# Optimization experiments

Hardware: AMD Instinct MI355X
Metric: run time of the kernel (lower is better)

## Reference

```python
import jax, jax.numpy as jnp
import numpy as np

N = 50000      # original nodes
DEG = 8        # regular out-degree
E = N * DEG    # edges
K = 2          # bloom factor per node
C = 25000      # clusters (new nodes)
D_IN = 128
D_OUT = 128
D_BLOOM = 16   # (lmax+1)^2, lmax=3
D_INTER = D_BLOOM + D_OUT


def seg_mean(vals, idx, num):
    # scatter_mean: segment_sum / counts (clipped to 1)
    s = jax.ops.segment_sum(vals, idx, num_segments=num)
    cnt = jax.ops.segment_sum(jnp.ones((idx.shape[0], 1), vals.dtype), idx, num_segments=num)
    return s / jnp.maximum(cnt, 1.0)


def setup_inputs() -> dict:
    key = jax.random.key(0)
    ks = jax.random.split(key, 10)
    x = jax.random.normal(ks[0], (N, D_IN), jnp.float32)
    pos = jax.random.normal(ks[1], (N, 3), jnp.float32)
    src = jnp.repeat(jnp.arange(N, dtype=jnp.int32), DEG)          # regular out-degree
    dst = jax.random.randint(ks[2], (E,), 0, N, jnp.int32)
    edge_index = jnp.stack([src, dst], axis=0)
    edge_attr = jax.random.normal(ks[3], (E, 3), jnp.float32)      # relative-position features
    batch = jnp.zeros((N,), jnp.int32)                              # single graph
    clusters = jax.random.randint(ks[4], (N * K,), 0, C, jnp.int32) # cluster assignment of bloom nodes
    W_conv = jax.random.normal(ks[5], (D_IN, D_INTER), jnp.float32) * 0.05
    W_cedge = jax.random.normal(ks[6], (3, D_INTER), jnp.float32) * 0.05
    W_bloom = jax.random.normal(ks[7], (D_BLOOM, K * 3), jnp.float32) * 0.05
    W_gather = jax.random.normal(ks[8], (D_OUT, D_OUT), jnp.float32) * 0.05
    W_gedge = jax.random.normal(ks[9], (3, D_OUT), jnp.float32) * 0.05
    return {"x": x, "pos": pos, "edge_index": edge_index, "edge_attr": edge_attr,
            "batch": batch, "clusters": clusters, "W_conv": W_conv, "W_cedge": W_cedge,
            "W_bloom": W_bloom, "W_gather": W_gather, "W_gedge": W_gedge}


def reference(x, pos, edge_index, edge_attr, batch, clusters,
              W_conv, W_cedge, W_bloom, W_gather, W_gedge):
    src, dst = edge_index[0], edge_index[1]
    # bloom conv: edge messages -> mean aggregate on destination
    msg = x[src] @ W_conv + edge_attr @ W_cedge                    # [E, D_INTER]
    out = seg_mean(msg, dst, N)                                    # [N, D_INTER]
    sph, h = out[:, :D_BLOOM], out[:, D_BLOOM:]
    # bloom-expand: each node emits K bloomed points
    bloom_batch = jnp.repeat(jnp.arange(N, dtype=jnp.int32), K)    # [N*K]
    bloom_pos = (pos[:, None, :] + (sph @ W_bloom).reshape(N, K, 3)).reshape(N * K, 3)
    # (bloom_pos feeds the external clusterer; `clusters` is its precomputed output)
    pos_b = pos[bloom_batch]                                       # [N*K, 3]
    new_pos = seg_mean(pos_b, clusters, C)                         # scatter_mean pool -> [C, 3]
    # gather conv over edges bloom-node -> cluster
    g_attr = pos_b - new_pos[clusters]                             # [N*K, 3]
    gmsg = h[bloom_batch] @ W_gather + g_attr @ W_gedge            # [N*K, D_OUT]
    x_new = seg_mean(gmsg, clusters, C)                            # [C, D_OUT]
    # new_edge_index: spspmm chain. For each original edge (a->b), node b's bloom
    # nodes map to clusters; clusters sharing a common neighbor a become connected.
    cb = clusters.reshape(N, K)[dst].reshape(N, DEG * K)           # [N, deg*K] (regular degree)
    dK = DEG * K
    ns = jnp.broadcast_to(cb[:, :, None], (N, dK, dK)).reshape(-1)
    nd = jnp.broadcast_to(cb[:, None, :], (N, dK, dK)).reshape(-1)
    enc = ns * C + nd                                              # fits int32 (C*C < 2^31)
    enc = jnp.unique(enc, size=enc.shape[0], fill_value=0)         # dedup like spspmm (padded with 0)
    new_edge_index = jnp.stack([enc // C, enc % C], axis=0)
    new_edge_attr = new_pos[new_edge_index[1]] - new_pos[new_edge_index[0]]
    return (x_new, new_pos, new_edge_index, new_edge_attr)
```

## Files before the change

kernel.cpp:

```cpp
#include <hip/hip_runtime.h>
#include <hip/hip_bf16.h>
#include <stdint.h>

#define N_NODES   50000
#define N_EDGES   400000
#define NK        100000
#define C_CL      25000
#define TOTE      12800000
#define CHUNK_BITS 18
#define NCHUNK    2385
#define HIST_BLOCKS 782

__global__ __launch_bounds__(256) void mm128(const float* __restrict__ A, int lda,
                                             const float* __restrict__ B, int ldb, int bcol0,
                                             float* __restrict__ out, int rows) {
    int t = blockIdx.x * 256 + threadIdx.x;
    int r = t >> 5;
    int c = (t & 31) << 2;
    if (r >= rows) return;
    const float* Ar = A + (size_t)r * lda;
    const float* Bc = B + bcol0 + c;
    float4 acc = make_float4(0.f, 0.f, 0.f, 0.f);
#pragma unroll
    for (int k = 0; k < 128; k += 4) {
        float4 a  = *(const float4*)(Ar + k);
        float4 b0 = *(const float4*)(Bc + (size_t)(k + 0) * ldb);
        float4 b1 = *(const float4*)(Bc + (size_t)(k + 1) * ldb);
        float4 b2 = *(const float4*)(Bc + (size_t)(k + 2) * ldb);
        float4 b3 = *(const float4*)(Bc + (size_t)(k + 3) * ldb);
        acc.x += a.x * b0.x + a.y * b1.x + a.z * b2.x + a.w * b3.x;
        acc.y += a.x * b0.y + a.y * b1.y + a.z * b2.y + a.w * b3.y;
        acc.z += a.x * b0.z + a.y * b1.z + a.z * b2.z + a.w * b3.z;
        acc.w += a.x * b0.w + a.y * b1.w + a.z * b2.w + a.w * b3.w;
    }
    *(float4*)(out + (size_t)r * 128 + c) = acc;
}

__global__ __launch_bounds__(256) void hist_idx(const int* __restrict__ idx, int n, int* __restrict__ cnt) {
    int i = blockIdx.x * 256 + threadIdx.x;
    if (i < n) atomicAdd(&cnt[idx[i]], 1);
}

__global__ __launch_bounds__(256) void reduce_blk(const int* __restrict__ v, int n, int* __restrict__ bsum) {
    __shared__ int s[256];
    int t = threadIdx.x;
    int i = blockIdx.x * 256 + t;
    s[t] = (i < n) ? v[i] : 0;
    __syncthreads();
    for (int o = 128; o > 0; o >>= 1) { if (t < o) s[t] += s[t + o]; __syncthreads(); }
    if (t == 0) bsum[blockIdx.x] = s[0];
}

__global__ __launch_bounds__(256) void scan_small(int* data, int n, int* total_out) {
    __shared__ int s[256];
    __shared__ int carry;
    int t = threadIdx.x;
    if (t == 0) carry = 0;
    __syncthreads();
    for (int base = 0; base < n; base += 256) {
        int i = base + t;
        int v = (i < n) ? data[i] : 0;
        s[t] = v;
        __syncthreads();
        for (int o = 1; o < 256; o <<= 1) {
            int x = (t >= o) ? s[t - o] : 0;
            __syncthreads();
            s[t] += x;
            __syncthreads();
        }
        int inc = s[t];
        int tot = s[255];
        int cy  = carry;
        __syncthreads();
        if (i < n) data[i] = cy + inc - v;
        if (t == 0) carry = cy + tot;
        __syncthreads();
    }
    if (t == 0 && total_out) *total_out = carry;
}

__global__ __launch_bounds__(256) void scan_offs(const int* __restrict__ cnt, int n,
                                                 const int* __restrict__ bscan, int* __restrict__ offs) {
    __shared__ int s[256];
    int t = threadIdx.x;
    int i = blockIdx.x * 256 + t;
    int v = (i < n) ? cnt[i] : 0;
    s[t] = v;
    __syncthreads();
    for (int o = 1; o < 256; o <<= 1) {
        int x = (t >= o) ? s[t - o] : 0;
        __syncthreads();
        s[t] += x;
        __syncthreads();
    }
    if (i < n) offs[i] = bscan[blockIdx.x] + s[t] - v;
}

__global__ __launch_bounds__(256) void scatter_ids(const int* __restrict__ idx, int n,
                                                   int* __restrict__ cursors, int* __restrict__ ids) {
    int i = blockIdx.x * 256 + threadIdx.x;
    if (i < n) {
        int p = atomicAdd(&cursors[idx[i]], 1);
        ids[p] = i;
    }
}

__global__ __launch_bounds__(256) void gather_h(const float* __restrict__ y, const float* __restrict__ ea,
                                                const int* __restrict__ offs, const int* __restrict__ cnt,
                                                const int* __restrict__ eids, const float* __restrict__ Wce,
                                                float* __restrict__ h) {
    int l = threadIdx.x & 63;
    int n = blockIdx.x * 4 + (threadIdx.x >> 6);
    int off = offs[n], m = cnt[n];
    float ax = 0.f, ay = 0.f, ae = 0.f;
    for (int i = 0; i < m; ++i) {
        int e = eids[off + i];
        int s = e >> 3;
        float2 v = *(const float2*)(y + (size_t)s * 128 + 2 * l);
        ax += v.x; ay += v.y;
        if (l < 3) ae += ea[(size_t)e * 3 + l];
    }
    float e0 = __shfl(ae, 0), e1 = __shfl(ae, 1), e2 = __shfl(ae, 2);
    float inv = 1.f / (float)(m > 0 ? m : 1);
    int c0 = 2 * l, c1 = 2 * l + 1;
    float h0 = (ax + e0 * Wce[16 + c0] + e1 * Wce[144 + 16 + c0] + e2 * Wce[288 + 16 + c0]) * inv;
    float h1 = (ay + e0 * Wce[16 + c1] + e1 * Wce[144 + 16 + c1] + e2 * Wce[288 + 16 + c1]) * inv;
    *(float2*)(h + (size_t)n * 128 + 2 * l) = make_float2(h0, h1);
}

__global__ __launch_bounds__(256) void gather_out(const float* __restrict__ hW, const float* __restrict__ pos,
                                                  const int* __restrict__ offs2, const int* __restrict__ cnt2,
                                                  const int* __restrict__ bids,
                                                  float* __restrict__ xnew, float* __restrict__ newpos) {
    int l = threadIdx.x & 63;
    int c = blockIdx.x * 4 + (threadIdx.x >> 6);
    int off = offs2[c], m = cnt2[c];
    float ax = 0.f, ay = 0.f, ap = 0.f;
    for (int i = 0; i < m; ++i) {
        int b  = bids[off + i];
        int nd = b >> 1;
        float2 v = *(const float2*)(hW + (size_t)nd * 128 + 2 * l);
        ax += v.x; ay += v.y;
        if (l < 3) ap += pos[(size_t)nd * 3 + l];
    }
    float inv = 1.f / (float)(m > 0 ? m : 1);
    *(float2*)(xnew + (size_t)c * 128 + 2 * l) = make_float2(ax * inv, ay * inv);
    if (l < 3) newpos[(size_t)c * 3 + l] = ap * inv;
}

__global__ __launch_bounds__(256) void pair_hist(const int* __restrict__ dstA, const int* __restrict__ clu,
                                                 int* __restrict__ gcnt) {
    __shared__ int cb[64][16];
    __shared__ int hist[NCHUNK];
    int t = threadIdx.x;
    int n0 = blockIdx.x * 64;
    int nvalid = N_NODES - n0; if (nvalid > 64) nvalid = 64;
    for (int i = t; i < NCHUNK; i += 256) hist[i] = 0;
    for (int i = t; i < 1024; i += 256) {
        int ln = i >> 4, j = i & 15;
        if (ln < nvalid) {
            int d = dstA[(n0 + ln) * 8 + (j >> 1)];
            cb[ln][j] = clu[d * 2 + (j & 1)];
        }
    }
    __syncthreads();
#pragma unroll 4
    for (int q = 0; q < 64; ++q) {
        int idx = t * 64 + q;
        int ln = idx >> 8, p = idx & 255;
        if (ln < nvalid) {
            unsigned enc = (unsigned)cb[ln][p >> 4] * 25000u + (unsigned)cb[ln][p & 15];
            atomicAdd(&hist[enc >> CHUNK_BITS], 1);
        }
    }
    __syncthreads();
    for (int i = t; i < NCHUNK; i += 256) { int h = hist[i]; if (h) atomicAdd(&gcnt[i], h); }
}

__global__ __launch_bounds__(256) void pair_scatter(const int* __restrict__ dstA, const int* __restrict__ clu,
                                                    int* __restrict__ gcur, unsigned* __restrict__ pbuf) {
    __shared__ int cb[64][16];
    __shared__ int hist[NCHUNK];
    __shared__ int lcur[NCHUNK];
    int t = threadIdx.x;
    int n0 = blockIdx.x * 64;
    int nvalid = N_NODES - n0; if (nvalid > 64) nvalid = 64;
    for (int i = t; i < NCHUNK; i += 256) hist[i] = 0;
    for (int i = t; i < 1024; i += 256) {
        int ln = i >> 4, j = i & 15;
        if (ln < nvalid) {
            int d = dstA[(n0 + ln) * 8 + (j >> 1)];
            cb[ln][j] = clu[d * 2 + (j & 1)];
        }
    }
    __syncthreads();
#pragma unroll 4
    for (int q = 0; q < 64; ++q) {
        int idx = t * 64 + q;
        int ln = idx >> 8, p = idx & 255;
        if (ln < nvalid) {
            unsigned enc = (unsigned)cb[ln][p >> 4] * 25000u + (unsigned)cb[ln][p & 15];
            atomicAdd(&hist[enc >> CHUNK_BITS], 1);
        }
    }
    __syncthreads();
    for (int i = t; i < NCHUNK; i += 256) { int h = hist[i]; if (h) lcur[i] = atomicAdd(&gcur[i], h); }
    __syncthreads();
#pragma unroll 4
    for (int q = 0; q < 64; ++q) {
        int idx = t * 64 + q;
        int ln = idx >> 8, p = idx & 255;
        if (ln < nvalid) {
            unsigned enc = (unsigned)cb[ln][p >> 4] * 25000u + (unsigned)cb[ln][p & 15];
            int pos = atomicAdd(&lcur[enc >> CHUNK_BITS], 1);
            pbuf[pos] = enc;
        }
    }
}

__global__ __launch_bounds__(256) void chunk_count(const unsigned* __restrict__ pbuf,
                                                   const int* __restrict__ goffs, const int* __restrict__ gcnt,
                                                   int* __restrict__ ucnt) {
    __shared__ unsigned bm[8192];
    __shared__ int s[256];
    int t = threadIdx.x, c = blockIdx.x;
    for (int i = t; i < 8192; i += 256) bm[i] = 0;
    __syncthreads();
    int off = goffs[c], m = gcnt[c];
    unsigned basee = (unsigned)c << CHUNK_BITS;
    for (int i = t; i < m; i += 256) {
        unsigned e = pbuf[off + i] - basee;
        atomicOr(&bm[e >> 5], 1u << (e & 31));
    }
    __syncthreads();
    int acc = 0;
#pragma unroll
    for (int w = 0; w < 32; ++w) acc += __popc(bm[w * 256 + t]);
    s[t] = acc;
    __syncthreads();
    for (int o = 128; o > 0; o >>= 1) { if (t < o) s[t] += s[t + o]; __syncthreads(); }
    if (t == 0) ucnt[c] = s[0];
}

__global__ __launch_bounds__(256) void chunk_emit(const unsigned* __restrict__ pbuf,
                                                  const int* __restrict__ goffs, const int* __restrict__ gcnt,
                                                  const int* __restrict__ uoffs, const float* __restrict__ newpos,
                                                  float* __restrict__ ei0, float* __restrict__ ei1,
                                                  float* __restrict__ attr) {
    __shared__ unsigned bm[8192];
    __shared__ int wsum[32][4];
    int t = threadIdx.x, c = blockIdx.x;
    int lane = t & 63, wid = t >> 6;
    for (int i = t; i < 8192; i += 256) bm[i] = 0;
    __syncthreads();
    int off = goffs[c], m = gcnt[c];
    unsigned basee = (unsigned)c << CHUNK_BITS;
    for (int i = t; i < m; i += 256) {
        unsigned e = pbuf[off + i] - basee;
        atomicOr(&bm[e >> 5], 1u << (e & 31));
    }
    __syncthreads();
    int ubase = uoffs[c];
    int carry = 0;
    for (int g = 0; g < 32; ++g) {
        unsigned word = bm[g * 256 + t];
        int pc = __popc(word);
        int incl = pc;
#pragma unroll
        for (int o = 1; o < 64; o <<= 1) {
            int v = __shfl_up(incl, o, 64);
            if (lane >= o) incl += v;
        }
        if (lane == 63) wsum[g][wid] = incl;
        __syncthreads();
        int w0 = wsum[g][0], w1 = wsum[g][1], w2 = wsum[g][2], w3 = wsum[g][3];
        int wpre = (wid > 0 ? w0 : 0) + (wid > 1 ? w1 : 0) + (wid > 2 ? w2 : 0);
        int rank = ubase + carry + wpre + incl - pc;
        carry += w0 + w1 + w2 + w3;
        unsigned wbase = basee + (((unsigned)(g * 256 + t)) << 5);
        while (word) {
            int b = __ffs(word) - 1;
            word &= word - 1;
            unsigned v  = wbase + (unsigned)b;
            unsigned ns = v / 25000u;
            unsigned nd = v - ns * 25000u;
            ei0[rank] = (float)ns;
            ei1[rank] = (float)nd;
            float dx = newpos[nd * 3 + 0] - newpos[ns * 3 + 0];
            float dy = newpos[nd * 3 + 1] - newpos[ns * 3 + 1];
            float dz = newpos[nd * 3 + 2] - newpos[ns * 3 + 2];
            attr[(size_t)3 * rank + 0] = dx;
            attr[(size_t)3 * rank + 1] = dy;
            attr[(size_t)3 * rank + 2] = dz;
            ++rank;
        }
    }
}

__global__ __launch_bounds__(256) void tail_zero(const int* __restrict__ Uptr,
                                                 float* __restrict__ ei0, float* __restrict__ ei1,
                                                 float* __restrict__ attr) {
    int i = blockIdx.x * 256 + threadIdx.x;
    if (i >= TOTE) return;
    if (i >= *Uptr) {
        ei0[i] = 0.f;
        ei1[i] = 0.f;
        attr[(size_t)3 * i + 0] = 0.f;
        attr[(size_t)3 * i + 1] = 0.f;
        attr[(size_t)3 * i + 2] = 0.f;
    }
}

extern "C" void kernel_launch(void* const* d_in, const int* in_sizes, int n_in,
                              void* d_out, int out_size, void* d_ws, size_t ws_size,
                              hipStream_t stream) {
    const float* x     = (const float*)d_in[0];
    const float* pos   = (const float*)d_in[1];
    const int*   dstA  = (const int*)d_in[2] + N_EDGES;
    const float* ea    = (const float*)d_in[3];
    const int*   clu   = (const int*)d_in[5];
    const float* Wconv = (const float*)d_in[6];
    const float* Wce   = (const float*)d_in[7];
    const float* Wg    = (const float*)d_in[9];

    float* out_f  = (float*)d_out;
    float* xnew   = out_f;
    float* newpos = out_f + 3200000;
    float* ei0    = out_f + 3275000;
    float* ei1    = out_f + 16075000;
    float* attr   = out_f + 28875000;
    float* y      = attr;
    float* h      = attr + 6400000;
    float* hW     = y;

    uint8_t* w8 = (uint8_t*)d_ws;
    unsigned* pbuf = (unsigned*)(w8);
    int* cnt       = (int*)(w8 + 51200000);
    int* offs      = (int*)(w8 + 51400000);
    int* cursors   = (int*)(w8 + 51600000);
    int* eids      = (int*)(w8 + 51800000);
    int* cnt2      = (int*)(w8 + 53400000);
    int* offs2     = (int*)(w8 + 53500000);
    int* cursors2  = (int*)(w8 + 53600000);
    int* bids      = (int*)(w8 + 53700000);
    int* bsum      = (int*)(w8 + 54100000);
    int* gcnt      = (int*)(w8 + 54120480);
    int* goffs     = (int*)(w8 + 54130020);
    int* gcur      = (int*)(w8 + 54139560);
    int* ucnt      = (int*)(w8 + 54149100);
    int* uoffs     = (int*)(w8 + 54158640);
    int* Uptr      = (int*)(w8 + 54168180);

    hipMemsetAsync(gcnt, 0, NCHUNK * 4, stream);
    hipMemsetAsync(cnt,  0, N_NODES * 4, stream);
    hipMemsetAsync(cnt2, 0, C_CL * 4, stream);

    mm128<<<(N_NODES * 32) / 256, 256, 0, stream>>>(x, 128, Wconv, 144, 16, y, N_NODES);

    hist_idx<<<(N_EDGES + 255) / 256, 256, 0, stream>>>(dstA, N_EDGES, cnt);
    reduce_blk<<<196, 256, 0, stream>>>(cnt, N_NODES, bsum);
    scan_small<<<1, 256, 0, stream>>>(bsum, 196, nullptr);
    scan_offs<<<196, 256, 0, stream>>>(cnt, N_NODES, bsum, offs);
    hipMemcpyAsync(cursors, offs, N_NODES * 4, hipMemcpyDeviceToDevice, stream);
    scatter_ids<<<(N_EDGES + 255) / 256, 256, 0, stream>>>(dstA, N_EDGES, cursors, eids);

    gather_h<<<N_NODES / 4, 256, 0, stream>>>(y, ea, offs, cnt, eids, Wce, h);

    mm128<<<(N_NODES * 32) / 256, 256, 0, stream>>>(h, 128, Wg, 128, 0, hW, N_NODES);

    hist_idx<<<(NK + 255) / 256, 256, 0, stream>>>(clu, NK, cnt2);
    reduce_blk<<<98, 256, 0, stream>>>(cnt2, C_CL, bsum);
    scan_small<<<1, 256, 0, stream>>>(bsum, 98, nullptr);
    scan_offs<<<98, 256, 0, stream>>>(cnt2, C_CL, bsum, offs2);
    hipMemcpyAsync(cursors2, offs2, C_CL * 4, hipMemcpyDeviceToDevice, stream);
    scatter_ids<<<(NK + 255) / 256, 256, 0, stream>>>(clu, NK, cursors2, bids);

    gather_out<<<C_CL / 4, 256, 0, stream>>>(hW, pos, offs2, cnt2, bids, xnew, newpos);

    pair_hist<<<HIST_BLOCKS, 256, 0, stream>>>(dstA, clu, gcnt);
    hipMemcpyAsync(goffs, gcnt, NCHUNK * 4, hipMemcpyDeviceToDevice, stream);
    scan_small<<<1, 256, 0, stream>>>(goffs, NCHUNK, nullptr);
    hipMemcpyAsync(gcur, goffs, NCHUNK * 4, hipMemcpyDeviceToDevice, stream);
    pair_scatter<<<HIST_BLOCKS, 256, 0, stream>>>(dstA, clu, gcur, pbuf);
    chunk_count<<<NCHUNK, 256, 0, stream>>>(pbuf, goffs, gcnt, ucnt);
    hipMemcpyAsync(uoffs, ucnt, NCHUNK * 4, hipMemcpyDeviceToDevice, stream);
    scan_small<<<1, 256, 0, stream>>>(uoffs, NCHUNK, Uptr);
    chunk_emit<<<NCHUNK, 256, 0, stream>>>(pbuf, goffs, gcnt, uoffs, newpos, ei0, ei1, attr);
    tail_zero<<<TOTE / 256, 256, 0, stream>>>(Uptr, ei0, ei1, attr);

    (void)in_sizes; (void)n_in; (void)out_size; (void)ws_size;
}
```

Baseline: 1.127 ms.

## Prefold W_gather into conv weights and compact deduped edges in place

Precomputes W1 = Wconv_h·Wg and W2 = Wce_h·Wg in a small kernel, so one 128x128 matmul over x replaces the conv matmul plus the second matmul on h. This relies on the linearity of the mean aggregation. It also merges the count and emit bitmap passes into one compaction kernel that writes the unique keys back into pbuf, followed by a flat expand kernel. That avoids building the shared-memory bitmap twice per chunk, at the cost of an extra global write and read of the compacted keys and a small change in floating-point summation order.

```diff
diff --git a/kernel.cpp b/kernel.cpp
--- a/kernel.cpp
+++ b/kernel.cpp
@@ -11,15 +11,35 @@
 #define NCHUNK    2385
 #define HIST_BLOCKS 782
 
+__global__ __launch_bounds__(256) void fuse_w(const float* __restrict__ Wconv, const float* __restrict__ Wce,
+                                              const float* __restrict__ Wg,
+                                              float* __restrict__ W1, float* __restrict__ W2) {
+    int id = blockIdx.x * 256 + threadIdx.x;
+    int r = id >> 7, c = id & 127;
+    if (r >= 131) return;
+    float acc = 0.f;
+    if (r < 128) {
+        const float* wr = Wconv + r * 144 + 16;
+#pragma unroll 8
+        for (int j = 0; j < 128; ++j) acc += wr[j] * Wg[j * 128 + c];
+        W1[r * 128 + c] = acc;
+    } else {
+        const float* wr = Wce + (r - 128) * 144 + 16;
+#pragma unroll 8
+        for (int j = 0; j < 128; ++j) acc += wr[j] * Wg[j * 128 + c];
+        W2[(r - 128) * 128 + c] = acc;
+    }
+}
+
 __global__ __launch_bounds__(256) void mm128(const float* __restrict__ A, int lda,
-                                             const float* __restrict__ B, int ldb, int bcol0,
+                                             const float* __restrict__ B, int ldb,
                                              float* __restrict__ out, int rows) {
     int t = blockIdx.x * 256 + threadIdx.x;
     int r = t >> 5;
     int c = (t & 31) << 2;
     if (r >= rows) return;
     const float* Ar = A + (size_t)r * lda;
-    const float* Bc = B + bcol0 + c;
+    const float* Bc = B + c;
     float4 acc = make_float4(0.f, 0.f, 0.f, 0.f);
 #pragma unroll
     for (int k = 0; k < 128; k += 4) {
@@ -105,10 +125,10 @@
     }
 }
 
-__global__ __launch_bounds__(256) void gather_h(const float* __restrict__ y, const float* __restrict__ ea,
-                                                const int* __restrict__ offs, const int* __restrict__ cnt,
-                                                const int* __restrict__ eids, const float* __restrict__ Wce,
-                                                float* __restrict__ h) {
+__global__ __launch_bounds__(256) void gather_hW(const float* __restrict__ yW, const float* __restrict__ ea,
+                                                 const int* __restrict__ offs, const int* __restrict__ cnt,
+                                                 const int* __restrict__ eids, const float* __restrict__ W2,
+                                                 float* __restrict__ hW) {
     int l = threadIdx.x & 63;
     int n = blockIdx.x * 4 + (threadIdx.x >> 6);
     int off = offs[n], m = cnt[n];
@@ -116,16 +136,16 @@
     for (int i = 0; i < m; ++i) {
         int e = eids[off + i];
         int s = e >> 3;
-        float2 v = *(const float2*)(y + (size_t)s * 128 + 2 * l);
+        float2 v = *(const float2*)(yW + (size_t)s * 128 + 2 * l);
         ax += v.x; ay += v.y;
         if (l < 3) ae += ea[(size_t)e * 3 + l];
     }
     float e0 = __shfl(ae, 0), e1 = __shfl(ae, 1), e2 = __shfl(ae, 2);
     float inv = 1.f / (float)(m > 0 ? m : 1);
     int c0 = 2 * l, c1 = 2 * l + 1;
-    float h0 = (ax + e0 * Wce[16 + c0] + e1 * Wce[144 + 16 + c0] + e2 * Wce[288 + 16 + c0]) * inv;
-    float h1 = (ay + e0 * Wce[16 + c1] + e1 * Wce[144 + 16 + c1] + e2 * Wce[288 + 16 + c1]) * inv;
-    *(float2*)(h + (size_t)n * 128 + 2 * l) = make_float2(h0, h1);
+    float h0 = (ax + e0 * W2[c0] + e1 * W2[128 + c0] + e2 * W2[256 + c0]) * inv;
+    float h1 = (ay + e0 * W2[c1] + e1 * W2[128 + c1] + e2 * W2[256 + c1]) * inv;
+    *(float2*)(hW + (size_t)n * 128 + 2 * l) = make_float2(h0, h1);
 }
 
 __global__ __launch_bounds__(256) void gather_out(const float* __restrict__ hW, const float* __restrict__ pos,
@@ -218,12 +238,13 @@
     }
 }
 
-__global__ __launch_bounds__(256) void chunk_count(const unsigned* __restrict__ pbuf,
-                                                   const int* __restrict__ goffs, const int* __restrict__ gcnt,
-                                                   int* __restrict__ ucnt) {
+__global__ __launch_bounds__(256) void chunk_compact(unsigned* __restrict__ pbuf,
+                                                     const int* __restrict__ goffs, const int* __restrict__ gcnt,
+                                                     int* __restrict__ ucnt) {
     __shared__ unsigned bm[8192];
-    __shared__ int s[256];
+    __shared__ int wsum[32][4];
     int t = threadIdx.x, c = blockIdx.x;
+    int lane = t & 63, wid = t >> 6;
     for (int i = t; i < 8192; i += 256) bm[i] = 0;
     __syncthreads();
     int off = goffs[c], m = gcnt[c];
@@ -233,34 +254,6 @@
         atomicOr(&bm[e >> 5], 1u << (e & 31));
     }
     __syncthreads();
-    int acc = 0;
-#pragma unroll
-    for (int w = 0; w < 32; ++w) acc += __popc(bm[w * 256 + t]);
-    s[t] = acc;
-    __syncthreads();
-    for (int o = 128; o > 0; o >>= 1) { if (t < o) s[t] += s[t + o]; __syncthreads(); }
-    if (t == 0) ucnt[c] = s[0];
-}
-
-__global__ __launch_bounds__(256) void chunk_emit(const unsigned* __restrict__ pbuf,
-                                                  const int* __restrict__ goffs, const int* __restrict__ gcnt,
-                                                  const int* __restrict__ uoffs, const float* __restrict__ newpos,
-                                                  float* __restrict__ ei0, float* __restrict__ ei1,
-                                                  float* __restrict__ attr) {
-    __shared__ unsigned bm[8192];
-    __shared__ int wsum[32][4];
-    int t = threadIdx.x, c = blockIdx.x;
-    int lane = t & 63, wid = t >> 6;
-    for (int i = t; i < 8192; i += 256) bm[i] = 0;
-    __syncthreads();
-    int off = goffs[c], m = gcnt[c];
-    unsigned basee = (unsigned)c << CHUNK_BITS;
-    for (int i = t; i < m; i += 256) {
-        unsigned e = pbuf[off + i] - basee;
-        atomicOr(&bm[e >> 5], 1u << (e & 31));
-    }
-    __syncthreads();
-    int ubase = uoffs[c];
     int carry = 0;
     for (int g = 0; g < 32; ++g) {
         unsigned word = bm[g * 256 + t];
@@ -275,25 +268,38 @@
         __syncthreads();
         int w0 = wsum[g][0], w1 = wsum[g][1], w2 = wsum[g][2], w3 = wsum[g][3];
         int wpre = (wid > 0 ? w0 : 0) + (wid > 1 ? w1 : 0) + (wid > 2 ? w2 : 0);
-        int rank = ubase + carry + wpre + incl - pc;
+        int rank = off + carry + wpre + incl - pc;
         carry += w0 + w1 + w2 + w3;
         unsigned wbase = basee + (((unsigned)(g * 256 + t)) << 5);
         while (word) {
             int b = __ffs(word) - 1;
             word &= word - 1;
-            unsigned v  = wbase + (unsigned)b;
-            unsigned ns = v / 25000u;
-            unsigned nd = v - ns * 25000u;
-            ei0[rank] = (float)ns;
-            ei1[rank] = (float)nd;
-            float dx = newpos[nd * 3 + 0] - newpos[ns * 3 + 0];
-            float dy = newpos[nd * 3 + 1] - newpos[ns * 3 + 1];
-            float dz = newpos[nd * 3 + 2] - newpos[ns * 3 + 2];
-            attr[(size_t)3 * rank + 0] = dx;
-            attr[(size_t)3 * rank + 1] = dy;
-            attr[(size_t)3 * rank + 2] = dz;
-            ++rank;
-        }
+            pbuf[rank++] = wbase + (unsigned)b;
+        }
+    }
+    if (t == 0) ucnt[c] = carry;
+}
+
+__global__ __launch_bounds__(256) void expand(const unsigned* __restrict__ pbuf,
+                                              const int* __restrict__ goffs, const int* __restrict__ ucnt,
+                                              const int* __restrict__ uoffs, const float* __restrict__ newpos,
+                                              float* __restrict__ ei0, float* __restrict__ ei1,
+                                              float* __restrict__ attr) {
+    int t = threadIdx.x, c = blockIdx.x;
+    int src = goffs[c], dst = uoffs[c], n = ucnt[c];
+    for (int j = t; j < n; j += 256) {
+        unsigned v  = pbuf[src + j];
+        unsigned ns = v / 25000u;
+        unsigned nd = v - ns * 25000u;
+        int o = dst + j;
+        ei0[o] = (float)ns;
+        ei1[o] = (float)nd;
+        float dx = newpos[nd * 3 + 0] - newpos[ns * 3 + 0];
+        float dy = newpos[nd * 3 + 1] - newpos[ns * 3 + 1];
+        float dz = newpos[nd * 3 + 2] - newpos[ns * 3 + 2];
+        attr[(size_t)3 * o + 0] = dx;
+        attr[(size_t)3 * o + 1] = dy;
+        attr[(size_t)3 * o + 2] = dz;
     }
 }
 
@@ -329,9 +335,8 @@
     float* ei0    = out_f + 3275000;
     float* ei1    = out_f + 16075000;
     float* attr   = out_f + 28875000;
-    float* y      = attr;
-    float* h      = attr + 6400000;
-    float* hW     = y;
+    float* yW     = attr;
+    float* hW     = attr + 6400000;
 
     uint8_t* w8 = (uint8_t*)d_ws;
     unsigned* pbuf = (unsigned*)(w8);
@@ -350,12 +355,16 @@
     int* ucnt      = (int*)(w8 + 54149100);
     int* uoffs     = (int*)(w8 + 54158640);
     int* Uptr      = (int*)(w8 + 54168180);
+    float* W1      = (float*)(w8 + 54200000);
+    float* W2      = (float*)(w8 + 54265536);
 
     hipMemsetAsync(gcnt, 0, NCHUNK * 4, stream);
     hipMemsetAsync(cnt,  0, N_NODES * 4, stream);
     hipMemsetAsync(cnt2, 0, C_CL * 4, stream);
 
-    mm128<<<(N_NODES * 32) / 256, 256, 0, stream>>>(x, 128, Wconv, 144, 16, y, N_NODES);
+    fuse_w<<<66, 256, 0, stream>>>(Wconv, Wce, Wg, W1, W2);
+
+    mm128<<<(N_NODES * 32) / 256, 256, 0, stream>>>(x, 128, W1, 128, yW, N_NODES);
 
     hist_idx<<<(N_EDGES + 255) / 256, 256, 0, stream>>>(dstA, N_EDGES, cnt);
     reduce_blk<<<196, 256, 0, stream>>>(cnt, N_NODES, bsum);
@@ -364,9 +373,7 @@
     hipMemcpyAsync(cursors, offs, N_NODES * 4, hipMemcpyDeviceToDevice, stream);
     scatter_ids<<<(N_EDGES + 255) / 256, 256, 0, stream>>>(dstA, N_EDGES, cursors, eids);
 
-    gather_h<<<N_NODES / 4, 256, 0, stream>>>(y, ea, offs, cnt, eids, Wce, h);
-
-    mm128<<<(N_NODES * 32) / 256, 256, 0, stream>>>(h, 128, Wg, 128, 0, hW, N_NODES);
+    gather_hW<<<N_NODES / 4, 256, 0, stream>>>(yW, ea, offs, cnt, eids, W2, hW);
 
     hist_idx<<<(NK + 255) / 256, 256, 0, stream>>>(clu, NK, cnt2);
     reduce_blk<<<98, 256, 0, stream>>>(cnt2, C_CL, bsum);
@@ -382,10 +389,10 @@
     scan_small<<<1, 256, 0, stream>>>(goffs, NCHUNK, nullptr);
     hipMemcpyAsync(gcur, goffs, NCHUNK * 4, hipMemcpyDeviceToDevice, stream);
     pair_scatter<<<HIST_BLOCKS, 256, 0, stream>>>(dstA, clu, gcur, pbuf);
-    chunk_count<<<NCHUNK, 256, 0, stream>>>(pbuf, goffs, gcnt, ucnt);
+    chunk_compact<<<NCHUNK, 256, 0, stream>>>(pbuf, goffs, gcnt, ucnt);
     hipMemcpyAsync(uoffs, ucnt, NCHUNK * 4, hipMemcpyDeviceToDevice, stream);
     scan_small<<<1, 256, 0, stream>>>(uoffs, NCHUNK, Uptr);
-    chunk_emit<<<NCHUNK, 256, 0, stream>>>(pbuf, goffs, gcnt, uoffs, newpos, ei0, ei1, attr);
+    expand<<<NCHUNK, 256, 0, stream>>>(pbuf, goffs, ucnt, uoffs, newpos, ei0, ei1, attr);
     tail_zero<<<TOTE / 256, 256, 0, stream>>>(Uptr, ei0, ei1, attr);
 
     (void)in_sizes; (void)n_in; (void)out_size; (void)ws_size;
```

New measurement: 984.4 us. 1.14x faster.
